# Kernel tuning notes

Measured on AMD Instinct MI355X. Metric: run time of the kernel, lower is better.

Reference implementation:

```python
import jax, jax.numpy as jnp
import numpy as np
import math

SPARSITY = 0.5
EPS = 1e-5


def _quant(x, bit, after_relu):
    # mirrors torch quantize_per_tensor math; straight-through (torch mutates x.data)
    def q(x):
        mx, mn = x.max(), x.min()
        scale = (mx - mn) / (2 ** bit - 1)
        if after_relu:
            ir = jnp.clip(jnp.round(x / scale), 0.0, 2 ** bit - 1)
            return ir * scale
        zp_min = jnp.floor(mn / scale)
        return (jnp.round((x - mn) / scale) + zp_min) * scale
    return x + jax.lax.stop_gradient(q(x) - x)


def _subnet(scores, k):
    # GetSubnet: top-k mask of |scores| with straight-through gradient
    s = jnp.abs(scores)
    flat = s.ravel()
    j = int((1.0 - k) * flat.size)
    order = jnp.argsort(flat)
    mask = jnp.zeros_like(flat).at[order[j:]].set(1.0).reshape(s.shape)
    return jax.lax.stop_gradient(mask - s) + s


def _scale(hw_one, fan_in):
    std = math.sqrt(2.0) / math.sqrt(fan_in * 0.5)
    return hw_one.mean() / std


def _blend_w(scores, sign, hw_one, hw_zero):
    m = _subnet(scores, SPARSITY)
    return sign * (hw_one[0] * m + hw_zero[0] * (1.0 - m))


def _conv(x, w):
    return jax.lax.conv_general_dilated(x, w, (1, 1), 'VALID',
                                        dimension_numbers=('NCHW', 'OIHW', 'NCHW'))


def _maxpool2(x):
    return jax.lax.reduce_window(x, -jnp.inf, jax.lax.max,
                                 (1, 1, 2, 2), (1, 1, 2, 2), 'VALID')


def _bn(x):
    m = x.mean((0, 2, 3), keepdims=True)
    v = x.var((0, 2, 3), keepdims=True)
    return (x - m) / jnp.sqrt(v + EPS)


def setup_inputs() -> dict:
    key = jax.random.key(0)
    ks = jax.random.split(key, 16)
    B = 4096
    shapes = {
        '1': (64, 1, 3, 3),
        '2': (16, 64, 3, 3),
        '3': (128, 400),
        '4': (10, 128),
    }
    inp = {'x': jax.random.normal(ks[0], (B, 1, 28, 28), dtype=jnp.float32)}
    i = 1
    for name, shp in shapes.items():
        inp['scores' + name] = jax.random.normal(ks[i], shp, dtype=jnp.float32); i += 1
        inp['sign' + name] = jnp.sign(jax.random.normal(ks[i], shp, dtype=jnp.float32)); i += 1
        inp['hw' + name + '_one'] = jax.random.uniform(ks[i], (1,) + shp, dtype=jnp.float32); i += 1
        # hw_zero: small "off" conductances
        inp['hw' + name + '_zero'] = 0.05 * jax.random.uniform(jax.random.fold_in(ks[i], 1), (1,) + shp, dtype=jnp.float32)
    inp['qb'] = 8
    return inp


def reference(x, scores1, sign1, hw1_one, hw1_zero,
              scores2, sign2, hw2_one, hw2_zero,
              scores3, sign3, hw3_one, hw3_zero,
              scores4, sign4, hw4_one, hw4_zero, qb):
    x = _maxpool2(x)
    x = _quant(x, qb, False)
    # conv1 (fan_in = 1*3*3 = 9)
    w1 = _blend_w(scores1, sign1, hw1_one, hw1_zero)
    x = _conv(x, w1) / _scale(hw1_one, 9)
    x = jax.nn.relu(_bn(x))
    x = _quant(x, qb, True)
    # conv2 (fan_in = 64*9 = 576)
    w2 = _blend_w(scores2, sign2, hw2_one, hw2_zero)
    x = _conv(x, w2) / _scale(hw2_one, 576)
    x = _maxpool2(x)
    x = jax.nn.relu(_bn(x))
    x = _quant(x, qb, True)
    x = x.reshape(x.shape[0], -1)  # [B, 400]
    # fc1 (fan_in = 400)
    w3 = _blend_w(scores3, sign3, hw3_one, hw3_zero)
    x = (x @ w3.T) / _scale(hw3_one, 400)
    x = jax.nn.relu(x)
    x = _quant(x, qb, True)
    # fc2 (fan_in = 128)
    w4 = _blend_w(scores4, sign4, hw4_one, hw4_zero)
    x = (x @ w4.T) / _scale(hw4_one, 128)
    return jax.nn.log_softmax(x, axis=1)
```

## Files before the change

kernel.cpp:

```cpp
#include <hip/hip_runtime.h>
#include <hip/hip_bf16.h>
#include <math.h>

#define DEV __device__ __forceinline__

constexpr int BATCH = 4096;
constexpr int NBA = 512;
constexpr int NBB = 4096;
constexpr int NBC = 4096;
constexpr int NBE = 512;
constexpr int NBW = 16;

constexpr size_t OFF_POOLED = 0;
constexpr size_t OFF_Y2P = OFF_POOLED + (size_t)BATCH*196;
constexpr size_t OFF_ST1 = OFF_Y2P;
constexpr size_t OFF_H3  = OFF_Y2P + (size_t)BATCH*400;
constexpr size_t OFF_ST2 = OFF_H3;
constexpr size_t OFF_W2  = OFF_H3 + (size_t)BATCH*128;
constexpr size_t OFF_W3  = OFF_W2 + 9216;
constexpr size_t OFF_W4  = OFF_W3 + 51200;
constexpr size_t OFF_WSC = OFF_W4 + 1280;
constexpr size_t OFF_BN1 = OFF_WSC + 4;
constexpr size_t OFF_BN2 = OFF_BN1 + 256;
constexpr size_t OFF_GMM = OFF_BN2 + 64;
constexpr size_t OFF_ONS = OFF_GMM + 8;
constexpr size_t OFF_T   = OFF_ONS + 16;
constexpr size_t OFF_MMA = OFF_T + 4;
constexpr size_t OFF_HIST= OFF_MMA + 1024;
constexpr size_t OFF_W1M = OFF_HIST + 32768;
constexpr size_t OFF_SEL = OFF_W1M + 2048;
constexpr size_t OFF_H2G = OFF_SEL + 8;
constexpr size_t OFF_H3G = OFF_H2G + 4096;

typedef __attribute__((ext_vector_type(8))) short bf16x8;
typedef __attribute__((ext_vector_type(4))) float f32x4;

struct InPtrs {
  const float* x;
  const float* sc[4];
  const float* sg[4];
  const float* on[4];
  const float* ze[4];
  const int* qb;
};

__constant__ const int KW_L[16]  ={0,1,1,2,2,2,2,2,2,2,2,2,2,2,2,3};
__constant__ const int KW_S[16]  ={0,0,1,0,1,2,3,4,5,6,7,8,9,10,11,0};
__constant__ const int KW_NB[4]  ={1,2,12,1};
__constant__ const int KW_N[4]   ={576,9216,51200,1280};
__constant__ const int KW_FAN[4] ={9,576,400,128};
__constant__ const int KW_BW0[4] ={0,1,3,15};
__constant__ const int KW_BW1[4] ={1,3,15,16};

DEV unsigned fenc(float f){ unsigned u=__float_as_uint(f); return (u&0x80000000u)? ~u : (u|0x80000000u); }
DEV float fdec(unsigned e){ return __uint_as_float((e&0x80000000u)? (e&0x7fffffffu) : ~e); }
DEV unsigned short f2bf(float f){ unsigned u=__float_as_uint(f); return (unsigned short)((u + 0x7fffu + ((u>>16)&1u))>>16); }

DEV float blk_sum(float v, float* red, int t){
  red[t]=v; __syncthreads();
  for (int s=128;s>0;s>>=1){ if(t<s) red[t]+=red[t+s]; __syncthreads(); }
  float r=red[0]; __syncthreads();
  return r;
}
DEV float blk_min(float v, float* red, int t){
  red[t]=v; __syncthreads();
  for (int s=128;s>0;s>>=1){ if(t<s) red[t]=fminf(red[t],red[t+s]); __syncthreads(); }
  float r=red[0]; __syncthreads();
  return r;
}
DEV float blk_max(float v, float* red, int t){
  red[t]=v; __syncthreads();
  for (int s=128;s>0;s>>=1){ if(t<s) red[t]=fmaxf(red[t],red[t+s]); __syncthreads(); }
  float r=red[0]; __syncthreads();
  return r;
}

DEV int2 find256(const int* hist, int nbins, int kk, int t, int* suf, int* sh2){
  const int G=nbins>>8;
  const int lo=t*G;
  int g=0;
  for (int b=0;b<G;++b) g+=hist[lo+b];
  suf[t]=g; __syncthreads();
  for (int s=1;s<256;s<<=1){
    int add=(t+s<256)?suf[t+s]:0;
    __syncthreads();
    suf[t]+=add;
    __syncthreads();
  }
  const int S=suf[t];
  const int Snext=(t<255)?suf[t+1]:0;
  if (S>=kk && Snext<kk){
    int c2=Snext;
    for (int b=lo+G-1;b>=lo;--b){
      c2+=hist[b];
      if (c2>=kk){ sh2[0]=b; sh2[1]=kk-(c2-hist[b]); break; }
    }
  }
  __syncthreads();
  int2 r=make_int2(sh2[0],sh2[1]);
  __syncthreads();
  return r;
}

DEV void build_pat(unsigned* PAT, const unsigned short* qxs, int t){
  for (int pos=t; pos<144; pos+=256){
    int py=(pos*171)>>11;
    int px=pos-py*12;
    const unsigned short* q0=qxs+py*16+px;
    unsigned e0=q0[0],  e1=q0[1],  e2=q0[2];
    unsigned e3=q0[16], e4=q0[17], e5=q0[18];
    unsigned e6=q0[32], e7=q0[33], e8=q0[34];
    uint4* dst=(uint4*)(PAT+pos*20);
    dst[0]=make_uint4(e0|(e1<<16), e2|(e3<<16), e4|(e5<<16), e6|(e7<<16));
    dst[1]=make_uint4(e8, 0u, 0u, 0u);
    dst[2]=make_uint4(0u,0u,0u,0u);
    dst[3]=make_uint4(0u,0u,0u,0u);
  }
}

__global__ __launch_bounds__(256) void ka_kernel(InPtrs in, float* __restrict__ ws){
  const int t=threadIdx.x, blk=blockIdx.x;
  __shared__ int h[2048];
  __shared__ float red[256];
  if (blk<NBA){
    if (blk==0){
      unsigned* Z=(unsigned*)(ws+OFF_H2G);
      for (int i=t;i<8192;i+=256) Z[i]=0u;
    }
    const float* x=in.x;
    float* pooled=ws+OFF_POOLED;
    float lmn=3.4e38f, lmx=-3.4e38f;
    for (int p=blk*256+t; p<BATCH*196; p+=NBA*256){
      int b=p/196, r=p-b*196;
      int oy=r/14, ox=r-oy*14;
      const float* px=x+b*784+oy*56+ox*2;
      float m=fmaxf(fmaxf(px[0],px[1]),fmaxf(px[28],px[29]));
      pooled[p]=m;
      lmn=fminf(lmn,m); lmx=fmaxf(lmx,m);
    }
    float bmn=blk_min(lmn,red,t);
    float bmx=blk_max(lmx,red,t);
    if (t==0){ ws[OFF_MMA+blk*2]=bmn; ws[OFF_MMA+blk*2+1]=bmx; }
  } else {
    const int bw=blk-NBA;
    const int L=KW_L[bw], s=KW_S[bw], nb=KW_NB[L];
    const int n4=KW_N[L]>>2;
    const int lo=(int)(((long long)n4*s)/nb), hi=(int)(((long long)n4*(s+1))/nb);
    const float4* sc4=(const float4*)in.sc[L];
    const float4* on4=(const float4*)in.on[L];
    for (int i=t;i<2048;i+=256) h[i]=0;
    __syncthreads();
    float onsum=0.f;
    for (int i=lo+t;i<hi;i+=256){
      float4 v=sc4[i];
      atomicAdd(&h[(__float_as_uint(v.x)&0x7fffffffu)>>20],1);
      atomicAdd(&h[(__float_as_uint(v.y)&0x7fffffffu)>>20],1);
      atomicAdd(&h[(__float_as_uint(v.z)&0x7fffffffu)>>20],1);
      atomicAdd(&h[(__float_as_uint(v.w)&0x7fffffffu)>>20],1);
      float4 o=on4[i];
      onsum+=(o.x+o.y)+(o.z+o.w);
    }
    __syncthreads();
    unsigned* GH=(unsigned*)(ws+OFF_HIST);
    for (int i=t;i<2048;i+=256) GH[bw*2048+i]=(unsigned)h[i];
    float S=blk_sum(onsum,red,t);
    if (t==0) ws[OFF_ONS+bw]=S;
  }
}

__global__ __launch_bounds__(256) void kw2a_kernel(float* __restrict__ ws){
  const int t=threadIdx.x, L=blockIdx.x;
  __shared__ int hist[2048];
  __shared__ int suf[256];
  __shared__ int sh2[2];
  __shared__ float redm[256], redx[256];
  if (L==0){
    float a0=ws[OFF_MMA+2*t],       a1=ws[OFF_MMA+2*(t+256)];
    float b0=ws[OFF_MMA+2*t+1],     b1=ws[OFF_MMA+2*(t+256)+1];
    redm[t]=fminf(a0,a1); redx[t]=fmaxf(b0,b1);
    __syncthreads();
    for (int s=128;s>0;s>>=1){
      if (t<s){ redm[t]=fminf(redm[t],redm[t+s]); redx[t]=fmaxf(redx[t],redx[t+s]); }
      __syncthreads();
    }
    unsigned* U=(unsigned*)(ws+OFF_GMM);
    if (t==0){ U[0]=fenc(redm[0]); U[1]=fenc(redx[0]); }
    if (t>=2 && t<8) U[t]=(t&1)? 0u : 0xFFFFFFFFu;
    unsigned* z=(unsigned*)(ws+OFF_W1M);
    for (int i=t;i<2048;i+=256) z[i]=0u;
    __syncthreads();
  }
  const unsigned* GH=(const unsigned*)(ws+OFF_HIST);
  for (int i=t;i<2048;i+=256){
    int s=0;
    for (int bw=KW_BW0[L]; bw<KW_BW1[L]; ++bw) s+=(int)GH[bw*2048+i];
    hist[i]=s;
  }
  __syncthreads();
  int2 f1=find256(hist,2048,KW_N[L]>>1,t,suf,sh2);
  if (t==0){
    unsigned* SEL=(unsigned*)(ws+OFF_SEL);
    SEL[L*2]=(unsigned)f1.x; SEL[L*2+1]=(unsigned)f1.y;
  }
}

__global__ __launch_bounds__(256) void kwp2_kernel(InPtrs in, float* __restrict__ ws){
  const int t=threadIdx.x, bw=blockIdx.x;
  const int L=KW_L[bw], s=KW_S[bw], nb=KW_NB[L];
  const int n4=KW_N[L]>>2;
  const int lo=(int)(((long long)n4*s)/nb), hi=(int)(((long long)n4*(s+1))/nb);
  const unsigned b0=((const unsigned*)(ws+OFF_SEL))[L*2];
  const float4* sc4=(const float4*)in.sc[L];
  unsigned* GH2=(unsigned*)(ws+OFF_H2G)+L*1024;
  for (int i=lo+t;i<hi;i+=256){
    float4 v=sc4[i];
    unsigned ux=__float_as_uint(v.x)&0x7fffffffu;
    unsigned uy=__float_as_uint(v.y)&0x7fffffffu;
    unsigned uz=__float_as_uint(v.z)&0x7fffffffu;
    unsigned uw=__float_as_uint(v.w)&0x7fffffffu;
    if ((ux>>20)==b0) atomicAdd(&GH2[(ux>>10)&1023u],1u);
    if ((uy>>20)==b0) atomicAdd(&GH2[(uy>>10)&1023u],1u);
    if ((uz>>20)==b0) atomicAdd(&GH2[(uz>>10)&1023u],1u);
    if ((uw>>20)==b0) atomicAdd(&GH2[(uw>>10)&1023u],1u);
  }
}

__global__ __launch_bounds__(256) void kwp3_kernel(InPtrs in, float* __restrict__ ws){
  const int t=threadIdx.x, bw=blockIdx.x;
  const int L=KW_L[bw], s=KW_S[bw], nb=KW_NB[L];
  const int n4=KW_N[L]>>2;
  const int lo=(int)(((long long)n4*s)/nb), hi=(int)(((long long)n4*(s+1))/nb);
  const unsigned* SEL=(const unsigned*)(ws+OFF_SEL);
  const unsigned b0=SEL[L*2]; const int r1=(int)SEL[L*2+1];
  __shared__ int hist[1024];
  __shared__ int suf[256];
  __shared__ int sh2[2];
  const unsigned* GH2=(const unsigned*)(ws+OFF_H2G)+L*1024;
  for (int i=t;i<1024;i+=256) hist[i]=(int)GH2[i];
  __syncthreads();
  int2 f2=find256(hist,1024,r1,t,suf,sh2);
  const unsigned pre=(b0<<10)|(unsigned)f2.x;
  const float4* sc4=(const float4*)in.sc[L];
  unsigned* GH3=(unsigned*)(ws+OFF_H3G)+L*1024;
  for (int i=lo+t;i<hi;i+=256){
    float4 v=sc4[i];
    unsigned ux=__float_as_uint(v.x)&0x7fffffffu;
    unsigned uy=__float_as_uint(v.y)&0x7fffffffu;
    unsigned uz=__float_as_uint(v.z)&0x7fffffffu;
    unsigned uw=__float_as_uint(v.w)&0x7fffffffu;
    if ((ux>>10)==pre) atomicAdd(&GH3[ux&1023u],1u);
    if ((uy>>10)==pre) atomicAdd(&GH3[uy&1023u],1u);
    if ((uz>>10)==pre) atomicAdd(&GH3[uz&1023u],1u);
    if ((uw>>10)==pre) atomicAdd(&GH3[uw&1023u],1u);
  }
}

__global__ __launch_bounds__(256) void kw3_kernel(InPtrs in, float* __restrict__ ws){
  const int t=threadIdx.x, bw=blockIdx.x;
  const int L=KW_L[bw], s=KW_S[bw], nb=KW_NB[L];
  const int n4=KW_N[L]>>2;
  const int lo=(int)(((long long)n4*s)/nb), hi=(int)(((long long)n4*(s+1))/nb);
  const unsigned* SEL=(const unsigned*)(ws+OFF_SEL);
  const unsigned b0=SEL[L*2]; const int r1=(int)SEL[L*2+1];
  __shared__ int hist[1024];
  __shared__ int suf[256];
  __shared__ int sh2[2];
  const unsigned* GH2=(const unsigned*)(ws+OFF_H2G)+L*1024;
  for (int i=t;i<1024;i+=256) hist[i]=(int)GH2[i];
  __syncthreads();
  int2 f2=find256(hist,1024,r1,t,suf,sh2);
  const unsigned pre=(b0<<10)|(unsigned)f2.x;
  const int r2=f2.y;
  __syncthreads();
  const unsigned* GH3=(const unsigned*)(ws+OFF_H3G)+L*1024;
  for (int i=t;i<1024;i+=256) hist[i]=(int)GH3[i];
  __syncthreads();
  int2 f3=find256(hist,1024,r2,t,suf,sh2);
  const unsigned T=(pre<<10)|(unsigned)f3.x;
  if (s==0 && t==0){
    float os=0.f;
    for (int b=KW_BW0[L]; b<KW_BW1[L]; ++b) os+=ws[OFF_ONS+b];
    ws[OFF_WSC+L]=(os/(float)KW_N[L])*sqrtf((float)KW_FAN[L])*0.5f;
  }
  const float4* sc4=(const float4*)in.sc[L];
  const float4* sg4=(const float4*)in.sg[L];
  const float4* on4=(const float4*)in.on[L];
  const float4* ze4=(const float4*)in.ze[L];
  float* wout=ws+OFF_W4;
  unsigned* W3Fu=(unsigned*)(ws+OFF_W3);
  unsigned short* W1F=(unsigned short*)(ws+OFF_W1M);
  unsigned short* W2F=(unsigned short*)(ws+OFF_W2);
  for (int i4=lo+t;i4<hi;i4+=256){
    float4 sv4=sc4[i4], g=sg4[i4], o=on4[i4], z=ze4[i4];
    float sv[4]={sv4.x,sv4.y,sv4.z,sv4.w}, gv[4]={g.x,g.y,g.z,g.w};
    float ov[4]={o.x,o.y,o.z,o.w}, zv[4]={z.x,z.y,z.z,z.w};
    #pragma unroll
    for (int j=0;j<4;++j){
      int i=i4*4+j;
      unsigned u=__float_as_uint(sv[j])&0x7fffffffu;
      float w=gv[j]*((u>=T)? ov[j] : zv[j]);
      if (L==0){
        int oc=i/9; int k=i-oc*9;
        int ocT=oc>>4, ocL=oc&15, quad=k>>3, kj=k&7;
        unsigned short hb=f2bf(w);
        float lo2=w-__uint_as_float((unsigned)hb<<16);
        W1F[((((ocT*2+0)*4+quad)*16+ocL)<<3)+kj]=hb;
        W1F[((((ocT*2+1)*4+quad)*16+ocL)<<3)+kj]=f2bf(lo2);
      } else if (L==1){
        int oc=i/576; int r=i-oc*576; int ic=r/9; int kp=r-ic*9;
        int ss=ic>>5, rem=ic&31, quad=rem>>3, kj=rem&7;
        unsigned short hb=f2bf(w);
        float lo2=w-__uint_as_float((unsigned)hb<<16);
        W2F[(((((kp*2+ss)*2+0)*4+quad)*16+oc)<<3)+kj]=hb;
        W2F[(((((kp*2+ss)*2+1)*4+quad)*16+oc)<<3)+kj]=f2bf(lo2);
      } else if (L==2){
        int oc=i/400; int kk=i-oc*400;
        unsigned short hb=f2bf(w);
        float lo2=w-__uint_as_float((unsigned)hb<<16);
        unsigned short lb=f2bf(lo2);
        int ct=oc>>4, l15=oc&15;
        unsigned idx=((unsigned)((kk>>4)*8+ct)*64u + (unsigned)(((kk>>2)&3)*16+l15))*4u + (unsigned)(kk&3);
        W3Fu[idx]=(unsigned)hb | ((unsigned)lb<<16);
      } else {
        wout[i]=w;
      }
    }
  }
}

__global__ __launch_bounds__(256) void kb_kernel(InPtrs in, const float* __restrict__ wsr, float* __restrict__ wsw){
  const int t=threadIdx.x, blk=blockIdx.x;
  __shared__ unsigned short qxs[256];
  __shared__ __align__(16) unsigned PAT[2880];
  __shared__ float xw[1024];
  const float* pooled=wsr+OFF_POOLED;
  const unsigned* U=(const unsigned*)(wsr+OFF_GMM);
  const float mn0=fdec(U[0]);
  const float mx0=fdec(U[1]);
  const float lvf=(float)((1<<in.qb[0])-1);
  const float s0=(mx0-mn0)/lvf, inv_s0=1.0f/s0, zp0=floorf(mn0/s0);
  const float sv=s0/wsr[OFF_WSC+0];
  if (t<224){
    int row=t>>4, col=t&15;
    float q=0.f;
    if (col<14){ float xx=pooled[(size_t)blk*196+row*14+col]; q=rintf((xx-mn0)*inv_s0)+zp0; }
    qxs[t]=(unsigned short)(__float_as_uint(q)>>16);
  }
  __syncthreads();
  build_pat(PAT,qxs,t);
  __syncthreads();
  {
    const int w=t>>6, lane=t&63;
    const int l15=lane&15, quad=lane>>4;
    const unsigned short* W1F=(const unsigned short*)(wsr+OFF_W1M);
    const unsigned short* PATu=(const unsigned short*)PAT;
    #pragma unroll
    for (int ocT=0; ocT<4; ++ocT){
      bf16x8 bh=*(const bf16x8*)(W1F+(((ocT*2+0)*64+lane)<<3));
      bf16x8 bl=*(const bf16x8*)(W1F+(((ocT*2+1)*64+lane)<<3));
      float sum=0.f,sq=0.f,mn=3.4e38f,mx=-3.4e38f;
      for (int tl=w; tl<9; tl+=4){
        bf16x8 a=*(const bf16x8*)(PATu+(tl*16+l15)*40+quad*8);
        f32x4 acc=(f32x4){0.f,0.f,0.f,0.f};
        acc=__builtin_amdgcn_mfma_f32_16x16x32_bf16(a,bh,acc,0,0,0);
        acc=__builtin_amdgcn_mfma_f32_16x16x32_bf16(a,bl,acc,0,0,0);
        #pragma unroll
        for (int r=0;r<4;++r){
          float v=acc[r]*sv;
          sum+=v; sq=fmaf(v,v,sq); mn=fminf(mn,v); mx=fmaxf(mx,v);
        }
      }
      #pragma unroll
      for (int d=16;d<64;d<<=1){
        sum+=__shfl_xor(sum,d);
        sq +=__shfl_xor(sq,d);
        mn=fminf(mn,__shfl_xor(mn,d));
        mx=fmaxf(mx,__shfl_xor(mx,d));
      }
      if (quad==0){
        float* p=xw+((w*4+ocT)*16+l15)*4;
        p[0]=sum; p[1]=sq; p[2]=mn; p[3]=mx;
      }
    }
  }
  __syncthreads();
  if (t<64){
    float sum=0.f,sq=0.f,mn=3.4e38f,mx=-3.4e38f;
    #pragma unroll
    for (int w=0;w<4;++w){
      const float* p=xw+((w*4+(t>>4))*16+(t&15))*4;
      sum+=p[0]; sq+=p[1]; mn=fminf(mn,p[2]); mx=fmaxf(mx,p[3]);
    }
    float* p=wsw+OFF_ST1+((size_t)t*NBB+blk)*4;
    p[0]=sum; p[1]=sq; p[2]=mn; p[3]=mx;
  }
}

__global__ __launch_bounds__(256) void kstat_kernel(const float* __restrict__ wsr, float* __restrict__ wsw,
                                                    unsigned long long inoff, int nparts, float Nf,
                                                    unsigned long long outoff, int mmslot){
  const int c=blockIdx.x, t=threadIdx.x;
  __shared__ float red[256];
  const float* p=wsr+inoff+(size_t)c*nparts*4;
  float sum=0.f,sq=0.f,mn=3.4e38f,mx=-3.4e38f;
  for (int i=t;i<nparts;i+=256){
    sum+=p[i*4]; sq+=p[i*4+1];
    mn=fminf(mn,p[i*4+2]); mx=fmaxf(mx,p[i*4+3]);
  }
  float S=blk_sum(sum,red,t);
  float Q=blk_sum(sq,red,t);
  float MN=blk_min(mn,red,t);
  float MX=blk_max(mx,red,t);
  if (t==0){
    float mean=S/Nf;
    float var=fmaxf(Q/Nf-mean*mean,0.f);
    float sd=sqrtf(var+1e-5f);
    float* o=wsw+outoff+c*4;
    float tmn=(MN-mean)/sd, tmx=(MX-mean)/sd;
    o[0]=mean; o[1]=sd; o[2]=tmn; o[3]=tmx;
    unsigned* U=(unsigned*)(wsw+OFF_GMM);
    atomicMin(&U[mmslot],fenc(tmn));
    atomicMax(&U[mmslot+1],fenc(tmx));
  }
}

__global__ __launch_bounds__(256) void kc_kernel(InPtrs in, const float* __restrict__ wsr, float* __restrict__ wsw){
  const int t=threadIdx.x, blk=blockIdx.x;
  __shared__ unsigned short qxs[256];
  __shared__ __align__(16) unsigned PATBUF[3328];
  __shared__ __align__(16) unsigned short actA[144*88];
  __shared__ float sA2[64], sB2[64];
  unsigned* PAT=PATBUF;
  float (*c2sP)[16][104]=(float(*)[16][104])PATBUF;
  const float* pooled=wsr+OFF_POOLED;
  const unsigned* U=(const unsigned*)(wsr+OFF_GMM);
  const float mn0=fdec(U[0]);
  const float mx0=fdec(U[1]);
  const float rmn=fdec(U[2]);
  const float rmx=fdec(U[3]);
  const float lvf=(float)((1<<in.qb[0])-1);
  const float s0=(mx0-mn0)/lvf, inv_s0=1.0f/s0, zp0=floorf(mn0/s0);
  const float s1w=wsr[OFF_WSC+0], s2w=wsr[OFF_WSC+1];
  const float s2=(fmaxf(rmx,0.f)-fmaxf(rmn,0.f))/lvf;
  const float inv_s2=1.0f/s2;
  const float g2=s2/s2w;
  if (t<64){
    float m=wsr[OFF_BN1+t*4], sd=wsr[OFF_BN1+t*4+1];
    sA2[t]=s0/(s1w*sd);
    sB2[t]=-m/sd;
  }
  if (t<224){
    int row=t>>4, col=t&15;
    float q=0.f;
    if (col<14){ float xx=pooled[(size_t)blk*196+row*14+col]; q=rintf((xx-mn0)*inv_s0)+zp0; }
    qxs[t]=(unsigned short)(__float_as_uint(q)>>16);
  }
  __syncthreads();
  build_pat(PAT,qxs,t);
  __syncthreads();
  const int w=t>>6, lane=t&63;
  const int l15=lane&15, quad=lane>>4;
  {
    const unsigned short* W1F=(const unsigned short*)(wsr+OFF_W1M);
    const unsigned short* PATu=(const unsigned short*)PAT;
    #pragma unroll
    for (int ocT=0; ocT<4; ++ocT){
      bf16x8 bh=*(const bf16x8*)(W1F+(((ocT*2+0)*64+lane)<<3));
      bf16x8 bl=*(const bf16x8*)(W1F+(((ocT*2+1)*64+lane)<<3));
      const int oc0=ocT*16+quad*4;
      const float a20=sA2[oc0],   b20=sB2[oc0];
      const float a21=sA2[oc0+1], b21=sB2[oc0+1];
      const float a22=sA2[oc0+2], b22=sB2[oc0+2];
      const float a23=sA2[oc0+3], b23=sB2[oc0+3];
      for (int tl=w; tl<9; tl+=4){
        bf16x8 a=*(const bf16x8*)(PATu+(tl*16+l15)*40+quad*8);
        f32x4 acc=(f32x4){0.f,0.f,0.f,0.f};
        acc=__builtin_amdgcn_mfma_f32_16x16x32_bf16(bh,a,acc,0,0,0);
        acc=__builtin_amdgcn_mfma_f32_16x16x32_bf16(bl,a,acc,0,0,0);
        const int pos=tl*16+l15;
        float f0=fminf(rintf(fmaxf(fmaf(acc[0],a20,b20),0.f)*inv_s2),lvf);
        float f1=fminf(rintf(fmaxf(fmaf(acc[1],a21,b21),0.f)*inv_s2),lvf);
        float f2v=fminf(rintf(fmaxf(fmaf(acc[2],a22,b22),0.f)*inv_s2),lvf);
        float f3=fminf(rintf(fmaxf(fmaf(acc[3],a23,b23),0.f)*inv_s2),lvf);
        unsigned w0=(__float_as_uint(f0)>>16)|((__float_as_uint(f1)>>16)<<16);
        unsigned w1=(__float_as_uint(f2v)>>16)|((__float_as_uint(f3)>>16)<<16);
        *(uint2*)(actA+pos*88+oc0)=make_uint2(w0,w1);
      }
    }
  }
  __syncthreads();
  {
    const int wm=w>>1, wk=w&1;
    const int k0=wk?5:0, nK=wk?4:5;
    const int nT2=wm?3:4;
    const unsigned short* W2F=(const unsigned short*)(wsr+OFF_W2);
    int abase[4];
    #pragma unroll
    for (int i=0;i<4;++i){
      int tau=wm*4+i;
      int posb=tau*16+l15;
      int pc=posb>99?99:posb;
      int py=pc/10, px=pc-py*10;
      abase[i]=(py*12+px)*176+quad*16;
    }
    f32x4 acc[4];
    acc[0]=(f32x4){0.f,0.f,0.f,0.f};
    acc[1]=(f32x4){0.f,0.f,0.f,0.f};
    acc[2]=(f32x4){0.f,0.f,0.f,0.f};
    acc[3]=(f32x4){0.f,0.f,0.f,0.f};
    const char* actB=(const char*)actA;
    #pragma unroll
    for (int kk=0;kk<5;++kk){
      if (kk<nK){
        int kykx=k0+kk;
        int ky=(kykx*11)>>5;
        int kx=kykx-ky*3;
        int co=(ky*12+kx)*176;
        #pragma unroll
        for (int s=0;s<2;++s){
          bf16x8 bh=*(const bf16x8*)(W2F+((((kykx*2+s)*2+0)*64+lane)<<3));
          bf16x8 bl=*(const bf16x8*)(W2F+((((kykx*2+s)*2+1)*64+lane)<<3));
          #pragma unroll
          for (int i=0;i<4;++i){
            if (i<nT2){
              bf16x8 a=*(const bf16x8*)(actB+abase[i]+co+s*64);
              acc[i]=__builtin_amdgcn_mfma_f32_16x16x32_bf16(a,bh,acc[i],0,0,0);
              acc[i]=__builtin_amdgcn_mfma_f32_16x16x32_bf16(a,bl,acc[i],0,0,0);
            }
          }
        }
      }
    }
    #pragma unroll
    for (int i=0;i<4;++i){
      if (i<nT2){
        int pos4=(wm*4+i)*16+quad*4;
        if (pos4<100){
          float4* dst=(float4*)&c2sP[wk][l15][pos4];
          *dst=make_float4(acc[i].x*g2,acc[i].y*g2,acc[i].z*g2,acc[i].w*g2);
        }
      }
    }
  }
  __syncthreads();
  {
    const int ch=t>>4, g=t&15;
    const float* cc0=&c2sP[0][ch][0];
    const float* cc1=&c2sP[1][ch][0];
    float sum=0.f,sq=0.f,mn=3.4e38f,mx=-3.4e38f;
    #pragma unroll
    for (int it=0;it<2;++it){
      int j=g+it*16;
      if (j<25){
        int py=(j*52)>>8;
        int px=j-py*5;
        int base=py*20+px*2;
        float2 p0=*(const float2*)(cc0+base);
        float2 p1=*(const float2*)(cc0+base+10);
        float2 q0=*(const float2*)(cc1+base);
        float2 q1=*(const float2*)(cc1+base+10);
        float a0=p0.x+q0.x, a1=p0.y+q0.y;
        float b0=p1.x+q1.x, b1=p1.y+q1.y;
        float v=fmaxf(fmaxf(a0,a1),fmaxf(b0,b1));
        wsw[OFF_Y2P+(size_t)blk*400+ch*25+j]=v;
        sum+=v; sq=fmaf(v,v,sq); mn=fminf(mn,v); mx=fmaxf(mx,v);
      }
    }
    #pragma unroll
    for (int d=1;d<16;d<<=1){
      sum+=__shfl_xor(sum,d);
      sq +=__shfl_xor(sq,d);
      mn=fminf(mn,__shfl_xor(mn,d));
      mx=fmaxf(mx,__shfl_xor(mx,d));
    }
    if (g==0){
      float* p=wsw+OFF_ST2+((size_t)ch*NBC+blk)*4;
      p[0]=sum; p[1]=sq; p[2]=mn; p[3]=mx;
    }
  }
}

__global__ __launch_bounds__(256) void ke_kernel(InPtrs in, const float* __restrict__ wsr, float* __restrict__ wsw){
  const int t=threadIdx.x, blk=blockIdx.x;
  __shared__ __align__(16) unsigned short xs[16*808];
  __shared__ float sm[16], sisd[16];
  __shared__ float rwn[4], rwx[4];
  const unsigned* U=(const unsigned*)(wsr+OFF_GMM);
  const float lvf=(float)((1<<in.qb[0])-1);
  const float rmn=fdec(U[4]);
  const float rmx=fdec(U[5]);
  if (t<16){ sm[t]=wsr[OFF_BN2+t*4]; sisd[t]=1.0f/wsr[OFF_BN2+t*4+1]; }
  const float s3=(fmaxf(rmx,0.f)-fmaxf(rmn,0.f))/lvf;
  const float inv_s3=1.0f/s3;
  const float inv_s3w=1.0f/wsr[OFF_WSC+2];
  const int b0=(blk>>1)*16;
  __syncthreads();
  {
    const int img=t>>4, tg=t&15;
    const float* yrow=wsr+OFF_Y2P+(size_t)(b0+img)*400;
    unsigned* xsu=(unsigned*)xs;
    for (int n=0;n<25;++n){
      int k=n*16+tg;
      int ch=k/25;
      float y=yrow[k];
      float r=fmaxf((y-sm[ch])*sisd[ch],0.f);
      float q=fminf(rintf(r*inv_s3),lvf);
      unsigned qb=__float_as_uint(q)>>16;
      xsu[img*404+k]=qb|(qb<<16);
    }
  }
  __syncthreads();
  const int w=t>>6, lane=t&63, l15=lane&15, quad=lane>>4;
  const int ct=(blk&1)*4+w;
  const bf16x8* Wf=(const bf16x8*)(wsr+OFF_W3);
  const unsigned short* arow=xs+l15*808;
  f32x4 acc=(f32x4){0.f,0.f,0.f,0.f};
  #pragma unroll 5
  for (int kt=0;kt<25;++kt){
    bf16x8 a=*(const bf16x8*)(arow+kt*32+quad*8);
    bf16x8 b=Wf[(kt*8+ct)*64+lane];
    acc=__builtin_amdgcn_mfma_f32_16x16x32_bf16(a,b,acc,0,0,0);
  }
  const float scale=s3*inv_s3w;
  float hmn=3.4e38f,hmx=-3.4e38f;
  #pragma unroll
  for (int r=0;r<4;++r){
    float h=fmaxf(acc[r]*scale,0.f);
    wsw[OFF_H3+(size_t)(b0+quad*4+r)*128+ct*16+l15]=h;
    hmn=fminf(hmn,h); hmx=fmaxf(hmx,h);
  }
  #pragma unroll
  for (int d=1;d<64;d<<=1){
    hmn=fminf(hmn,__shfl_xor(hmn,d));
    hmx=fmaxf(hmx,__shfl_xor(hmx,d));
  }
  if (lane==0){ rwn[w]=hmn; rwx[w]=hmx; }
  __syncthreads();
  if (t==0){
    float mn=fminf(fminf(rwn[0],rwn[1]),fminf(rwn[2],rwn[3]));
    float mx=fmaxf(fmaxf(rwx[0],rwx[1]),fmaxf(rwx[2],rwx[3]));
    float* p=wsw+OFF_MMA+(size_t)blk*2;
    p[0]=mn; p[1]=mx;
  }
}

__global__ __launch_bounds__(256) void kf_kernel(InPtrs in, const float* __restrict__ wsr, float* __restrict__ out){
  const int t=threadIdx.x, blk=blockIdx.x;
  __shared__ float w4s[1280];
  __shared__ float redn[256], redxs[256];
  const float lvf=(float)((1<<in.qb[0])-1);
  for (int i=t;i<1280;i+=256) w4s[i]=wsr[OFF_W4+i];
  {
    const float* mmp=wsr+OFF_MMA;
    float mn=3.4e38f, mx=-3.4e38f;
    for (int i=t;i<NBE;i+=256){
      mn=fminf(mn,mmp[2*i]);
      mx=fmaxf(mx,mmp[2*i+1]);
    }
    redn[t]=mn; redxs[t]=mx;
    __syncthreads();
    for (int s=128;s>0;s>>=1){
      if (t<s){ redn[t]=fminf(redn[t],redn[t+s]); redxs[t]=fmaxf(redxs[t],redxs[t+s]); }
      __syncthreads();
    }
  }
  const float hmn=redn[0];
  const float hmx=redxs[0];
  const float s4=(hmx-hmn)/lvf;
  const float inv_s4=1.0f/s4;
  const float inv_s4w=1.0f/wsr[OFF_WSC+3];
  const int row=blk*64+(t>>2), l4=t&3;
  const float4* hr4=(const float4*)(wsr+OFF_H3+(size_t)row*128);
  float acc[10];
  #pragma unroll
  for (int j=0;j<10;++j) acc[j]=0.f;
  #pragma unroll 2
  for (int j=0;j<8;++j){
    float4 v=hr4[l4*8+j];
    int kb=(l4*8+j)*4;
    float q0=fminf(rintf(v.x*inv_s4),lvf)*s4;
    float q1=fminf(rintf(v.y*inv_s4),lvf)*s4;
    float q2=fminf(rintf(v.z*inv_s4),lvf)*s4;
    float q3=fminf(rintf(v.w*inv_s4),lvf)*s4;
    #pragma unroll
    for (int o=0;o<10;++o){
      const float* wr=w4s+o*128+kb;
      acc[o]=fmaf(q0,wr[0],acc[o]);
      acc[o]=fmaf(q1,wr[1],acc[o]);
      acc[o]=fmaf(q2,wr[2],acc[o]);
      acc[o]=fmaf(q3,wr[3],acc[o]);
    }
  }
  #pragma unroll
  for (int o=0;o<10;++o){
    acc[o]+=__shfl_xor(acc[o],1);
    acc[o]+=__shfl_xor(acc[o],2);
  }
  if (l4==0){
    float mx=-3.4e38f;
    #pragma unroll
    for (int o=0;o<10;++o){ acc[o]*=inv_s4w; mx=fmaxf(mx,acc[o]); }
    float se=0.f;
    #pragma unroll
    for (int o=0;o<10;++o) se+=expf(acc[o]-mx);
    const float ls=logf(se);
    #pragma unroll
    for (int o=0;o<10;++o) out[row*10+o]=acc[o]-mx-ls;
  }
}

extern "C" void kernel_launch(void* const* d_in, const int* in_sizes, int n_in,
                              void* d_out, int out_size, void* d_ws, size_t ws_size,
                              hipStream_t stream){
  (void)in_sizes; (void)n_in; (void)out_size; (void)ws_size;
  InPtrs P;
  P.x=(const float*)d_in[0];
  for (int l=0;l<4;++l){
    P.sc[l]=(const float*)d_in[1+l*4];
    P.sg[l]=(const float*)d_in[2+l*4];
    P.on[l]=(const float*)d_in[3+l*4];
    P.ze[l]=(const float*)d_in[4+l*4];
  }
  P.qb=(const int*)d_in[17];
  float* ws=(float*)d_ws;

  hipLaunchKernelGGL(ka_kernel,   dim3(NBA+NBW), dim3(256), 0, stream, P, ws);
  hipLaunchKernelGGL(kw2a_kernel, dim3(4),       dim3(256), 0, stream, ws);
  hipLaunchKernelGGL(kwp2_kernel, dim3(NBW),     dim3(256), 0, stream, P, ws);
  hipLaunchKernelGGL(kwp3_kernel, dim3(NBW),     dim3(256), 0, stream, P, ws);
  hipLaunchKernelGGL(kw3_kernel,  dim3(NBW),     dim3(256), 0, stream, P, ws);
  hipLaunchKernelGGL(kb_kernel,   dim3(NBB),     dim3(256), 0, stream, P, ws, ws);
  hipLaunchKernelGGL(kstat_kernel, dim3(64), dim3(256), 0, stream, ws, ws,
                     (unsigned long long)OFF_ST1, NBB, 4096.f*144.f, (unsigned long long)OFF_BN1, 2);
  hipLaunchKernelGGL(kc_kernel,   dim3(NBC),     dim3(256), 0, stream, P, ws, ws);
  hipLaunchKernelGGL(kstat_kernel, dim3(16), dim3(256), 0, stream, ws, ws,
                     (unsigned long long)OFF_ST2, NBC, 4096.f*25.f, (unsigned long long)OFF_BN2, 4);
  hipLaunchKernelGGL(ke_kernel,   dim3(NBE),     dim3(256), 0, stream, P, ws, ws);
  hipLaunchKernelGGL(kf_kernel,   dim3(64),      dim3(256), 0, stream, P, ws, (float*)d_out);
}
```

Baseline: 232.8 us.

## Batch images per block in pooling and conv1-stat kernels, fold scales

The conv1 statistics kernel now processes four images per block (grid cut from 4096 to 1024), keeping the weight fragments in registers and deferring the scale multiply and the cross-lane reduction to the end. The pooling kernel gives each block eight whole images with a fixed thread-to-pixel mapping instead of a grid-stride loop with divisions. The inverse quantization scale is folded into the BN affine coefficients, and a divide by 25 is replaced by a multiply-shift. The aim is to cut launch and per-block overhead and redundant arithmetic, in exchange for fewer blocks and more registers per thread.

```diff
diff --git a/kernel.cpp b/kernel.cpp
--- a/kernel.cpp
+++ b/kernel.cpp
@@ -6,7 +6,7 @@
 
 constexpr int BATCH = 4096;
 constexpr int NBA = 512;
-constexpr int NBB = 4096;
+constexpr int NBB = 1024;
 constexpr int NBC = 4096;
 constexpr int NBE = 512;
 constexpr int NBW = 16;
@@ -130,13 +130,17 @@
     const float* x=in.x;
     float* pooled=ws+OFF_POOLED;
     float lmn=3.4e38f, lmx=-3.4e38f;
-    for (int p=blk*256+t; p<BATCH*196; p+=NBA*256){
-      int b=p/196, r=p-b*196;
-      int oy=r/14, ox=r-oy*14;
-      const float* px=x+b*784+oy*56+ox*2;
-      float m=fmaxf(fmaxf(px[0],px[1]),fmaxf(px[28],px[29]));
-      pooled[p]=m;
-      lmn=fminf(lmn,m); lmx=fmaxf(lmx,m);
+    if (t<196){
+      const int oy=(t*2341)>>15;
+      const int ox=t-oy*14;
+      const float* xb=x+(size_t)blk*8*784+oy*56+ox*2;
+      #pragma unroll
+      for (int im=0; im<8; ++im){
+        const float* px=xb+im*784;
+        float m=fmaxf(fmaxf(px[0],px[1]),fmaxf(px[28],px[29]));
+        pooled[(size_t)(blk*8+im)*196+t]=m;
+        lmn=fminf(lmn,m); lmx=fmaxf(lmx,m);
+      }
     }
     float bmn=blk_min(lmn,red,t);
     float bmx=blk_max(lmx,red,t);
@@ -340,59 +344,70 @@
   const float lvf=(float)((1<<in.qb[0])-1);
   const float s0=(mx0-mn0)/lvf, inv_s0=1.0f/s0, zp0=floorf(mn0/s0);
   const float sv=s0/wsr[OFF_WSC+0];
-  if (t<224){
-    int row=t>>4, col=t&15;
-    float q=0.f;
-    if (col<14){ float xx=pooled[(size_t)blk*196+row*14+col]; q=rintf((xx-mn0)*inv_s0)+zp0; }
-    qxs[t]=(unsigned short)(__float_as_uint(q)>>16);
-  }
-  __syncthreads();
-  build_pat(PAT,qxs,t);
-  __syncthreads();
-  {
-    const int w=t>>6, lane=t&63;
-    const int l15=lane&15, quad=lane>>4;
-    const unsigned short* W1F=(const unsigned short*)(wsr+OFF_W1M);
+  const int w=t>>6, lane=t&63, l15=lane&15, quad=lane>>4;
+  const unsigned short* W1F=(const unsigned short*)(wsr+OFF_W1M);
+  bf16x8 bh[4], bl[4];
+  #pragma unroll
+  for (int ocT=0; ocT<4; ++ocT){
+    bh[ocT]=*(const bf16x8*)(W1F+(((ocT*2+0)*64+lane)<<3));
+    bl[ocT]=*(const bf16x8*)(W1F+(((ocT*2+1)*64+lane)<<3));
+  }
+  float sum[4], sq[4], mn[4], mx[4];
+  #pragma unroll
+  for (int i=0;i<4;++i){ sum[i]=0.f; sq[i]=0.f; mn[i]=3.4e38f; mx[i]=-3.4e38f; }
+  for (int img=0; img<4; ++img){
+    if (t<224){
+      int row=t>>4, col=t&15;
+      float q=0.f;
+      if (col<14){ float xx=pooled[(size_t)(blk*4+img)*196+row*14+col]; q=rintf((xx-mn0)*inv_s0)+zp0; }
+      qxs[t]=(unsigned short)(__float_as_uint(q)>>16);
+    }
+    __syncthreads();
+    build_pat(PAT,qxs,t);
+    __syncthreads();
     const unsigned short* PATu=(const unsigned short*)PAT;
     #pragma unroll
     for (int ocT=0; ocT<4; ++ocT){
-      bf16x8 bh=*(const bf16x8*)(W1F+(((ocT*2+0)*64+lane)<<3));
-      bf16x8 bl=*(const bf16x8*)(W1F+(((ocT*2+1)*64+lane)<<3));
-      float sum=0.f,sq=0.f,mn=3.4e38f,mx=-3.4e38f;
       for (int tl=w; tl<9; tl+=4){
         bf16x8 a=*(const bf16x8*)(PATu+(tl*16+l15)*40+quad*8);
         f32x4 acc=(f32x4){0.f,0.f,0.f,0.f};
-        acc=__builtin_amdgcn_mfma_f32_16x16x32_bf16(a,bh,acc,0,0,0);
-        acc=__builtin_amdgcn_mfma_f32_16x16x32_bf16(a,bl,acc,0,0,0);
+        acc=__builtin_amdgcn_mfma_f32_16x16x32_bf16(a,bh[ocT],acc,0,0,0);
+        acc=__builtin_amdgcn_mfma_f32_16x16x32_bf16(a,bl[ocT],acc,0,0,0);
         #pragma unroll
         for (int r=0;r<4;++r){
-          float v=acc[r]*sv;
-          sum+=v; sq=fmaf(v,v,sq); mn=fminf(mn,v); mx=fmaxf(mx,v);
+          float v=acc[r];
+          sum[ocT]+=v; sq[ocT]=fmaf(v,v,sq[ocT]);
+          mn[ocT]=fminf(mn[ocT],v); mx[ocT]=fmaxf(mx[ocT],v);
         }
       }
-      #pragma unroll
-      for (int d=16;d<64;d<<=1){
-        sum+=__shfl_xor(sum,d);
-        sq +=__shfl_xor(sq,d);
-        mn=fminf(mn,__shfl_xor(mn,d));
-        mx=fmaxf(mx,__shfl_xor(mx,d));
-      }
-      if (quad==0){
-        float* p=xw+((w*4+ocT)*16+l15)*4;
-        p[0]=sum; p[1]=sq; p[2]=mn; p[3]=mx;
-      }
+    }
+    __syncthreads();
+  }
+  #pragma unroll
+  for (int ocT=0; ocT<4; ++ocT){
+    float s=sum[ocT], q2=sq[ocT], a=mn[ocT], b=mx[ocT];
+    #pragma unroll
+    for (int d=16;d<64;d<<=1){
+      s+=__shfl_xor(s,d);
+      q2+=__shfl_xor(q2,d);
+      a=fminf(a,__shfl_xor(a,d));
+      b=fmaxf(b,__shfl_xor(b,d));
+    }
+    if (quad==0){
+      float* p=xw+((w*4+ocT)*16+l15)*4;
+      p[0]=s; p[1]=q2; p[2]=a; p[3]=b;
     }
   }
   __syncthreads();
   if (t<64){
-    float sum=0.f,sq=0.f,mn=3.4e38f,mx=-3.4e38f;
-    #pragma unroll
-    for (int w=0;w<4;++w){
-      const float* p=xw+((w*4+(t>>4))*16+(t&15))*4;
-      sum+=p[0]; sq+=p[1]; mn=fminf(mn,p[2]); mx=fmaxf(mx,p[3]);
+    float s=0.f,q2=0.f,a=3.4e38f,b=-3.4e38f;
+    #pragma unroll
+    for (int w2=0;w2<4;++w2){
+      const float* p=xw+((w2*4+(t>>4))*16+(t&15))*4;
+      s+=p[0]; q2+=p[1]; a=fminf(a,p[2]); b=fmaxf(b,p[3]);
     }
     float* p=wsw+OFF_ST1+((size_t)t*NBB+blk)*4;
-    p[0]=sum; p[1]=sq; p[2]=mn; p[3]=mx;
+    p[0]=s*sv; p[1]=q2*sv*sv; p[2]=a*sv; p[3]=b*sv;
   }
 }
 
@@ -446,8 +461,8 @@
   const float g2=s2/s2w;
   if (t<64){
     float m=wsr[OFF_BN1+t*4], sd=wsr[OFF_BN1+t*4+1];
-    sA2[t]=s0/(s1w*sd);
-    sB2[t]=-m/sd;
+    sA2[t]=s0/(s1w*sd)*inv_s2;
+    sB2[t]=(-m/sd)*inv_s2;
   }
   if (t<224){
     int row=t>>4, col=t&15;
@@ -478,10 +493,10 @@
         acc=__builtin_amdgcn_mfma_f32_16x16x32_bf16(bh,a,acc,0,0,0);
         acc=__builtin_amdgcn_mfma_f32_16x16x32_bf16(bl,a,acc,0,0,0);
         const int pos=tl*16+l15;
-        float f0=fminf(rintf(fmaxf(fmaf(acc[0],a20,b20),0.f)*inv_s2),lvf);
-        float f1=fminf(rintf(fmaxf(fmaf(acc[1],a21,b21),0.f)*inv_s2),lvf);
-        float f2v=fminf(rintf(fmaxf(fmaf(acc[2],a22,b22),0.f)*inv_s2),lvf);
-        float f3=fminf(rintf(fmaxf(fmaf(acc[3],a23,b23),0.f)*inv_s2),lvf);
+        float f0=fminf(rintf(fmaxf(fmaf(acc[0],a20,b20),0.f)),lvf);
+        float f1=fminf(rintf(fmaxf(fmaf(acc[1],a21,b21),0.f)),lvf);
+        float f2v=fminf(rintf(fmaxf(fmaf(acc[2],a22,b22),0.f)),lvf);
+        float f3=fminf(rintf(fmaxf(fmaf(acc[3],a23,b23),0.f)),lvf);
         unsigned w0=(__float_as_uint(f0)>>16)|((__float_as_uint(f1)>>16)<<16);
         unsigned w1=(__float_as_uint(f2v)>>16)|((__float_as_uint(f3)>>16)<<16);
         *(uint2*)(actA+pos*88+oc0)=make_uint2(w0,w1);
@@ -601,7 +616,7 @@
     unsigned* xsu=(unsigned*)xs;
     for (int n=0;n<25;++n){
       int k=n*16+tg;
-      int ch=k/25;
+      int ch=(k*5243)>>17;
       float y=yrow[k];
       float r=fmaxf((y-sm[ch])*sisd[ch],0.f);
       float q=fminf(rintf(r*inv_s3),lvf);
```

New measurement: 230.7 us. Within noise of the previous version (-0.9%).
